# Performance work log

Hardware: AMD Instinct MI355X
Metric: run time of the kernel (lower is better)

The kernel has to match this reference:

```python
import jax, jax.numpy as jnp
import numpy as np

N_ENTITIES = 100000
N_EDGES = 500000
N_RELATIONS = 200
DIM = 64
HEADS = 4
POW_ITER = 5
ALPHA = 0.1
LEAKY_SLOPE = 0.01
EPS = 1e-16


def setup_inputs() -> dict:
    key = jax.random.key(0)
    ks = jax.random.split(key, 11)
    scale = 0.1
    return {
        "entity_embed": jax.random.normal(ks[0], (N_ENTITIES, DIM), jnp.float32),
        "relation_embed": jax.random.normal(ks[1], (N_RELATIONS, DIM), jnp.float32),
        "W_h": jax.random.normal(ks[2], (DIM, HEADS * DIM), jnp.float32) * scale,
        "W_t": jax.random.normal(ks[3], (DIM, HEADS * DIM), jnp.float32) * scale,
        "W_r": jax.random.normal(ks[4], (DIM, HEADS * DIM), jnp.float32) * scale,
        "att_h": jax.random.normal(ks[5], (HEADS, DIM), jnp.float32) * scale,
        "att_t": jax.random.normal(ks[6], (HEADS, DIM), jnp.float32) * scale,
        "att_r": jax.random.normal(ks[7], (HEADS, DIM), jnp.float32) * scale,
        "W_o": jax.random.normal(ks[8], (HEADS * DIM, DIM), jnp.float32) * scale,
        "edge_index": jax.random.randint(ks[9], (2, N_EDGES), 0, N_ENTITIES, jnp.int64),
        "edge_type": jax.random.randint(ks[10], (N_EDGES,), 0, N_RELATIONS, jnp.int64),
    }


def _segment_softmax(scores, seg_ids, num_segments):
    # scores: [E, heads]; softmax over edges sharing the same seg_id, per head
    m = jax.ops.segment_max(scores, seg_ids, num_segments=num_segments)
    e = jnp.exp(scores - m[seg_ids])
    denom = jax.ops.segment_sum(e, seg_ids, num_segments=num_segments)
    return e / (denom[seg_ids] + EPS)


def reference(entity_embed, relation_embed, W_h, W_t, W_r,
              att_h, att_t, att_r, W_o, edge_index, edge_type):
    head_ids, tail_ids = edge_index[0], edge_index[1]

    # per-edge gathered embeddings, projected per head: [E, heads, dim]
    Wh = (entity_embed[head_ids] @ W_h).reshape(-1, HEADS, DIM)
    Wt = (entity_embed[tail_ids] @ W_t).reshape(-1, HEADS, DIM)
    Wr = (relation_embed[edge_type] @ W_r).reshape(-1, HEADS, DIM)

    s_h = jnp.sum(jnp.tanh(Wh) * att_h[None], axis=-1)  # [E, heads]
    s_t = jnp.sum(jnp.tanh(Wt) * att_t[None], axis=-1)
    s_r = jnp.sum(jnp.tanh(Wr) * att_r[None], axis=-1)
    scores = jax.nn.leaky_relu(s_h + s_t + s_r, negative_slope=LEAKY_SLOPE)

    att = _segment_softmax(scores, head_ids, N_ENTITIES)  # [E, heads]
    A = (1.0 - ALPHA) * att

    # PPR power iteration, vectorized over heads: Z: [N, heads, dim]
    Z0 = entity_embed[:, None, :]  # [N, 1, dim]
    Z_init = jnp.broadcast_to(Z0, (N_ENTITIES, HEADS, DIM))

    def step(Z, _):
        msgs = A[:, :, None] * Z[tail_ids]  # [E, heads, dim]
        Z_new = jax.ops.segment_sum(msgs, head_ids, num_segments=N_ENTITIES) + ALPHA * Z0
        return Z_new, None

    Z, _ = jax.lax.scan(step, Z_init, None, length=POW_ITER)

    out = Z.reshape(N_ENTITIES, HEADS * DIM) @ W_o  # [N, dim]
    return out
```

## Files before the change

kernel.cpp:

```cpp
#include <hip/hip_runtime.h>
#include <hip/hip_fp16.h>
#include <math.h>

#define N_ENT 100000
#define N_EDGE 500000
#define N_REL 200

typedef short bf16x8 __attribute__((ext_vector_type(8)));
typedef _Float16 f16x8 __attribute__((ext_vector_type(8)));
typedef float f32x4 __attribute__((ext_vector_type(4)));

__device__ __forceinline__ float fast_tanh(float x) {
    float xc = fminf(x, 15.f);
    float e = __expf(2.f * xc);
    return 1.f - 2.f * __builtin_amdgcn_rcpf(e + 1.f);
}

__device__ __forceinline__ unsigned short f2bf(float f) {
    unsigned u = __float_as_uint(f);
    unsigned r = u + 0x7FFF + ((u >> 16) & 1);
    return (unsigned short)(r >> 16);
}

__device__ __forceinline__ uint2 pack_half4(const float4 v) {
    __half2 lo = __floats2half2_rn(v.x, v.y);
    __half2 hi = __floats2half2_rn(v.z, v.w);
    uint2 r;
    r.x = *reinterpret_cast<const unsigned int*>(&lo);
    r.y = *reinterpret_cast<const unsigned int*>(&hi);
    return r;
}

__device__ __forceinline__ float4 unpack_half4(uint2 u) {
    __half2 lo = *reinterpret_cast<const __half2*>(&u.x);
    __half2 hi = *reinterpret_cast<const __half2*>(&u.y);
    float2 a = __half22float2(lo);
    float2 b = __half22float2(hi);
    return make_float4(a.x, a.y, b.x, b.y);
}

__global__ __launch_bounds__(256) void cvt_emb_kernel(
    const float* __restrict__ in, unsigned short* __restrict__ out, int nquads)
{
    for (int i = blockIdx.x * 256 + threadIdx.x; i < nquads; i += gridDim.x * 256) {
        float4 v = ((const float4*)in)[i];
        ushort4 o;
        o.x = f2bf(v.x); o.y = f2bf(v.y); o.z = f2bf(v.z); o.w = f2bf(v.w);
        ((ushort4*)out)[i] = o;
    }
}

__global__ __launch_bounds__(256) void cvt_wT_kernel(
    const float* __restrict__ W0, const float* __restrict__ W1,
    unsigned short* __restrict__ wT)
{
    int idx = blockIdx.x * 256 + threadIdx.x;
    if (idx >= 2 * 256 * 64) return;
    int mat = idx >> 14;
    int rem = idx & 16383;
    int col = rem >> 6;
    int k   = rem & 63;
    const float* W = (mat == 0) ? W0 : W1;
    wT[idx] = f2bf(W[k * 256 + col]);
}

__global__ __launch_bounds__(256) void cvt_woT_kernel(
    const float* __restrict__ Wo, __half* __restrict__ woT)
{
    int idx = blockIdx.x * 256 + threadIdx.x;
    if (idx >= 64 * 256) return;
    int d = idx >> 8;
    int k = idx & 255;
    woT[idx] = __float2half(Wo[k * 64 + d]);
}

__global__ __launch_bounds__(256) void proj_mfma_kernel(
    const unsigned short* __restrict__ emb_bf,
    const unsigned short* __restrict__ wT,
    const float* __restrict__ att0, const float* __restrict__ att1,
    float* __restrict__ p0, float* __restrict__ p1, int nrows)
{
    const int wv   = threadIdx.x >> 6;
    const int lane = threadIdx.x & 63;
    const int r4   = lane >> 4;
    const int cl   = lane & 15;
    const int rowbase = blockIdx.x * 64 + wv * 16;

    int ra = min(rowbase + cl, nrows - 1);
    bf16x8 a0 = *(const bf16x8*)(emb_bf + (size_t)ra * 64 + 8 * r4);
    bf16x8 a1 = *(const bf16x8*)(emb_bf + (size_t)ra * 64 + 8 * r4 + 32);

#pragma unroll
    for (int mat = 0; mat < 2; ++mat) {
        const float* att = (mat == 0) ? att0 : att1;
        float* p         = (mat == 0) ? p0 : p1;
        float pacc[4][4];
#pragma unroll
        for (int head = 0; head < 4; ++head) {
            float vsum[4] = {0.f, 0.f, 0.f, 0.f};
#pragma unroll
            for (int sub = 0; sub < 4; ++sub) {
                int col = head * 64 + sub * 16 + cl;
                const unsigned short* wp =
                    wT + ((size_t)(mat * 256 + col)) * 64 + 8 * r4;
                bf16x8 b0 = *(const bf16x8*)(wp);
                bf16x8 b1 = *(const bf16x8*)(wp + 32);
                f32x4 c = {0.f, 0.f, 0.f, 0.f};
                c = __builtin_amdgcn_mfma_f32_16x16x32_bf16(a0, b0, c, 0, 0, 0);
                c = __builtin_amdgcn_mfma_f32_16x16x32_bf16(a1, b1, c, 0, 0, 0);
                float av = att[head * 64 + sub * 16 + cl];
#pragma unroll
                for (int j = 0; j < 4; ++j)
                    vsum[j] = fmaf(fast_tanh(c[j]), av, vsum[j]);
            }
#pragma unroll
            for (int j = 0; j < 4; ++j) {
                float v = vsum[j];
                v += __shfl_xor(v, 1, 64);
                v += __shfl_xor(v, 2, 64);
                v += __shfl_xor(v, 4, 64);
                v += __shfl_xor(v, 8, 64);
                pacc[head][j] = v;
            }
        }
        if (cl == 0) {
#pragma unroll
            for (int j = 0; j < 4; ++j) {
                int row = rowbase + r4 * 4 + j;
                if (row < nrows) {
                    *(float4*)(p + (size_t)row * 4) = make_float4(
                        pacc[0][j], pacc[1][j], pacc[2][j], pacc[3][j]);
                }
            }
        }
    }
}

__global__ __launch_bounds__(256) void proj_gemm_kernel(
    const float* __restrict__ emb,
    const float* __restrict__ W0,
    const float* __restrict__ att0,
    float* __restrict__ p0,
    int nrows)
{
    __shared__ float e_lds[64][68];
    __shared__ float w0_lds[64][64];
    __shared__ float red[4][4][64];

    const int t    = threadIdx.x;
    const int wv   = t >> 6;
    const int lane = t & 63;
    const int er   = t & 15;
    const int d0   = (t >> 4) * 4;
    const int base = blockIdx.x * 64;

#pragma unroll
    for (int i = 0; i < 4; ++i) {
        int f = t + 256 * i;
        int row = f >> 4, c4 = f & 15;
        int gr = min(base + row, nrows - 1);
        float4 v = *(const float4*)(emb + (size_t)gr * 64 + 4 * c4);
        *(float4*)&e_lds[row][4 * c4] = v;
    }

    float p0s[4][4];

    for (int head = 0; head < 4; ++head) {
        {
            int k0 = t >> 4, c4 = t & 15;
#pragma unroll
            for (int kk = 0; kk < 4; ++kk) {
                int k = k0 + 16 * kk;
                *(float4*)&w0_lds[k][4 * c4] =
                    *(const float4*)(W0 + (size_t)k * 256 + head * 64 + 4 * c4);
            }
        }
        __syncthreads();

        float acc0[4][4] = {};
        for (int k4 = 0; k4 < 16; ++k4) {
            float4 z0 = *(const float4*)&e_lds[er +  0][4 * k4];
            float4 z1 = *(const float4*)&e_lds[er + 16][4 * k4];
            float4 z2 = *(const float4*)&e_lds[er + 32][4 * k4];
            float4 z3 = *(const float4*)&e_lds[er + 48][4 * k4];
            const float zr[4][4] = {
                {z0.x, z0.y, z0.z, z0.w},
                {z1.x, z1.y, z1.z, z1.w},
                {z2.x, z2.y, z2.z, z2.w},
                {z3.x, z3.y, z3.z, z3.w}};
#pragma unroll
            for (int jj = 0; jj < 4; ++jj) {
                float4 w0v = *(const float4*)&w0_lds[4 * k4 + jj][d0];
#pragma unroll
                for (int i = 0; i < 4; ++i) {
                    float zj = zr[i][jj];
                    acc0[i][0] = fmaf(zj, w0v.x, acc0[i][0]);
                    acc0[i][1] = fmaf(zj, w0v.y, acc0[i][1]);
                    acc0[i][2] = fmaf(zj, w0v.z, acc0[i][2]);
                    acc0[i][3] = fmaf(zj, w0v.w, acc0[i][3]);
                }
            }
        }

        float4 av0 = *(const float4*)(att0 + head * 64 + d0);
#pragma unroll
        for (int i = 0; i < 4; ++i) {
            float v = fast_tanh(acc0[i][0]) * av0.x
                    + fast_tanh(acc0[i][1]) * av0.y
                    + fast_tanh(acc0[i][2]) * av0.z
                    + fast_tanh(acc0[i][3]) * av0.w;
            v += __shfl_xor(v, 16, 64);
            v += __shfl_xor(v, 32, 64);
            p0s[head][i] = v;
        }
        __syncthreads();
    }

    if (lane < 16) {
#pragma unroll
        for (int h = 0; h < 4; ++h)
#pragma unroll
            for (int i = 0; i < 4; ++i)
                red[wv][h][lane + 16 * i] = p0s[h][i];
    }
    __syncthreads();
    if (t < 64) {
        int row = base + t;
        if (row < nrows) {
            float4 pv;
            pv.x = red[0][0][t] + red[1][0][t] + red[2][0][t] + red[3][0][t];
            pv.y = red[0][1][t] + red[1][1][t] + red[2][1][t] + red[3][1][t];
            pv.z = red[0][2][t] + red[1][2][t] + red[2][2][t] + red[3][2][t];
            pv.w = red[0][3][t] + red[1][3][t] + red[2][3][t] + red[3][3][t];
            *(float4*)(p0 + (size_t)row * 4) = pv;
        }
    }
}

__global__ __launch_bounds__(256) void hist_kernel(
    const int* __restrict__ eidx, int* __restrict__ counts)
{
    int e = blockIdx.x * 256 + threadIdx.x;
    if (e >= N_EDGE) return;
    atomicAdd(&counts[eidx[e]], 1);
}

__global__ __launch_bounds__(1024) void scan_kernel(
    const int* __restrict__ counts, int* __restrict__ row_start)
{
    __shared__ int wsum[16];
    __shared__ int carry_s;
    const int lane = threadIdx.x & 63;
    const int wid  = threadIdx.x >> 6;
    if (threadIdx.x == 0) carry_s = 0;
    __syncthreads();
    for (int base = 0; base < N_ENT; base += 4096) {
        int i0 = base + (int)threadIdx.x * 4;
        int4 v = make_int4(0, 0, 0, 0);
        if (i0 + 3 < N_ENT) v = *(const int4*)(counts + i0);
        else {
            if (i0 + 0 < N_ENT) v.x = counts[i0 + 0];
            if (i0 + 1 < N_ENT) v.y = counts[i0 + 1];
            if (i0 + 2 < N_ENT) v.z = counts[i0 + 2];
            if (i0 + 3 < N_ENT) v.w = counts[i0 + 3];
        }
        int s1 = v.x + v.y, s2 = s1 + v.z, tsum = s2 + v.w;
        int incl = tsum;
#pragma unroll
        for (int off = 1; off < 64; off <<= 1) {
            int t = __shfl_up(incl, off, 64);
            if (lane >= off) incl += t;
        }
        if (lane == 63) wsum[wid] = incl;
        __syncthreads();
        int wave_off = 0;
#pragma unroll
        for (int w = 0; w < 16; ++w)
            wave_off += (w < wid) ? wsum[w] : 0;
        int carry = carry_s;
        int excl = carry + wave_off + (incl - tsum);
        if (i0 + 3 < N_ENT) {
            *(int4*)(row_start + i0) = make_int4(excl, excl + v.x, excl + s1, excl + s2);
        } else {
            if (i0 + 0 < N_ENT) row_start[i0 + 0] = excl;
            if (i0 + 1 < N_ENT) row_start[i0 + 1] = excl + v.x;
            if (i0 + 2 < N_ENT) row_start[i0 + 2] = excl + s1;
            if (i0 + 3 < N_ENT) row_start[i0 + 3] = excl + s2;
        }
        __syncthreads();
        if (threadIdx.x == 1023) carry_s = carry + wave_off + incl;
    }
    __syncthreads();
    if (threadIdx.x == 0) row_start[N_ENT] = carry_s;
}

__global__ __launch_bounds__(256) void scatter_score_kernel(
    const int* __restrict__ eidx, const int* __restrict__ etype,
    const float* __restrict__ ph, const float* __restrict__ pt,
    const float* __restrict__ pr,
    const int* __restrict__ row_start, int* __restrict__ cursor,
    int* __restrict__ csr_col, float* __restrict__ csr_a)
{
    int e = blockIdx.x * 256 + threadIdx.x;
    if (e >= N_EDGE) return;
    int hn = eidx[e];
    int tn = eidx[N_EDGE + e];
    int r  = etype[e];
    float4 a = *(const float4*)(ph + (size_t)hn * 4);
    float4 b = *(const float4*)(pt + (size_t)tn * 4);
    float4 c = *(const float4*)(pr + (size_t)r * 4);
    float s0 = a.x + b.x + c.x;
    float s1 = a.y + b.y + c.y;
    float s2 = a.z + b.z + c.z;
    float s3 = a.w + b.w + c.w;
    s0 = s0 >= 0.f ? s0 : 0.01f * s0;
    s1 = s1 >= 0.f ? s1 : 0.01f * s1;
    s2 = s2 >= 0.f ? s2 : 0.01f * s2;
    s3 = s3 >= 0.f ? s3 : 0.01f * s3;
    float4 ev = make_float4(__expf(s0), __expf(s1), __expf(s2), __expf(s3));
    int pos = row_start[hn] + atomicAdd(&cursor[hn], 1);
    csr_col[pos] = tn;
    *(float4*)(csr_a + (size_t)pos * 4) = ev;
}

__global__ __launch_bounds__(256) void normalize_kernel(
    const int* __restrict__ row_start, float* __restrict__ csr_a)
{
    const int wid  = threadIdx.x >> 6;
    const int lane = threadIdx.x & 63;
    const int n = blockIdx.x * 4 + wid;
    if (n >= N_ENT) return;
    const int s   = row_start[n];
    const int end = row_start[n + 1];
    const int nf  = (end - s) * 4;

    float sum = 0.f;
    for (int f = lane; f < nf; f += 64)
        sum += csr_a[(size_t)s * 4 + f];
#pragma unroll
    for (int off = 4; off < 64; off <<= 1)
        sum += __shfl_xor(sum, off, 64);
    float scale = 0.9f * __builtin_amdgcn_rcpf(sum + 1e-16f);
    for (int f = lane; f < nf; f += 64)
        csr_a[(size_t)s * 4 + f] *= scale;
}

template <bool IN_HALF>
__device__ __forceinline__ float4 spmm_row(
    int n, int lane, int h,
    const __half* __restrict__ Zin_h, const float* __restrict__ emb,
    const int* __restrict__ row_start, const int* __restrict__ csr_col,
    const float* __restrict__ csr_a)
{
    const float4* e4 = (const float4*)emb;
    float4 zi = e4[(size_t)n * 16 + (lane & 15)];
    float4 acc0 = make_float4(0.1f * zi.x, 0.1f * zi.y, 0.1f * zi.z, 0.1f * zi.w);
    float4 acc1 = make_float4(0.f, 0.f, 0.f, 0.f);
    float4 acc2 = make_float4(0.f, 0.f, 0.f, 0.f);
    float4 acc3 = make_float4(0.f, 0.f, 0.f, 0.f);

    const int s   = row_start[n];
    const int end = row_start[n + 1];

    auto zrow = [&](int c) -> float4 {
        if (IN_HALF) {
            uint2 u = *(const uint2*)(Zin_h + (size_t)c * 256 + 4 * lane);
            return unpack_half4(u);
        } else {
            return *(const float4*)(emb + (size_t)c * 64 + 4 * (lane & 15));
        }
    };
    auto fma4 = [](float4& acc, float a, const float4& z) {
        acc.x = fmaf(a, z.x, acc.x);
        acc.y = fmaf(a, z.y, acc.y);
        acc.z = fmaf(a, z.z, acc.z);
        acc.w = fmaf(a, z.w, acc.w);
    };

    for (int b = s; b < end; b += 16) {
        const int nb = min(16, end - b);
        int   cl = (lane < nb) ? csr_col[b + lane] : 0;
        float al = (lane < nb * 4) ? csr_a[(size_t)b * 4 + lane] : 0.f;

        int j = 0;
        for (; j + 4 <= nb; j += 4) {
            int c0 = __shfl(cl, j + 0, 64);
            int c1 = __shfl(cl, j + 1, 64);
            int c2 = __shfl(cl, j + 2, 64);
            int c3 = __shfl(cl, j + 3, 64);
            float a0 = __shfl(al, (j + 0) * 4 + h, 64);
            float a1 = __shfl(al, (j + 1) * 4 + h, 64);
            float a2 = __shfl(al, (j + 2) * 4 + h, 64);
            float a3 = __shfl(al, (j + 3) * 4 + h, 64);
            float4 za = zrow(c0);
            float4 zb = zrow(c1);
            float4 zc = zrow(c2);
            float4 zd = zrow(c3);
            fma4(acc0, a0, za);
            fma4(acc1, a1, zb);
            fma4(acc2, a2, zc);
            fma4(acc3, a3, zd);
        }
        if (j + 0 < nb) {
            int c = __shfl(cl, j + 0, 64);
            float a = __shfl(al, (j + 0) * 4 + h, 64);
            fma4(acc0, a, zrow(c));
        }
        if (j + 1 < nb) {
            int c = __shfl(cl, j + 1, 64);
            float a = __shfl(al, (j + 1) * 4 + h, 64);
            fma4(acc1, a, zrow(c));
        }
        if (j + 2 < nb) {
            int c = __shfl(cl, j + 2, 64);
            float a = __shfl(al, (j + 2) * 4 + h, 64);
            fma4(acc2, a, zrow(c));
        }
    }
    acc0.x += acc1.x + acc2.x + acc3.x;
    acc0.y += acc1.y + acc2.y + acc3.y;
    acc0.z += acc1.z + acc2.z + acc3.z;
    acc0.w += acc1.w + acc2.w + acc3.w;
    return acc0;
}

template <bool IN_HALF>
__global__ __launch_bounds__(256) void spmm_kernel(
    const void* __restrict__ Zin_v, const float* __restrict__ emb,
    const int* __restrict__ row_start, const int* __restrict__ csr_col,
    const float* __restrict__ csr_a, void* __restrict__ Zout_v)
{
    const int wave = threadIdx.x >> 6;
    const int lane = threadIdx.x & 63;
    const int n = blockIdx.x * 4 + wave;
    const int h = lane >> 4;
    float4 acc = spmm_row<IN_HALF>(n, lane, h, (const __half*)Zin_v, emb,
                                   row_start, csr_col, csr_a);
    *(uint2*)((__half*)Zout_v + (size_t)n * 256 + 4 * lane) = pack_half4(acc);
}

__global__ __launch_bounds__(256) void spmm_out_fused_kernel(
    const __half* __restrict__ Zin, const float* __restrict__ emb,
    const int* __restrict__ row_start, const int* __restrict__ csr_col,
    const float* __restrict__ csr_a,
    const __half* __restrict__ woT,
    float* __restrict__ out)
{
    __shared__ _Float16 zl[16][264];
    const int wv   = threadIdx.x >> 6;
    const int lane = threadIdx.x & 63;
    const int h    = lane >> 4;
    const int base = blockIdx.x * 16;

#pragma unroll
    for (int rr = 0; rr < 4; ++rr) {
        int n = base + wv * 4 + rr;
        float4 acc = spmm_row<true>(n, lane, h, Zin, emb,
                                    row_start, csr_col, csr_a);
        *(uint2*)&zl[wv * 4 + rr][4 * lane] = pack_half4(acc);
    }
    __syncthreads();

    const int cl = lane & 15;
    const int r4 = lane >> 4;
    f16x8 a[8];
#pragma unroll
    for (int ks = 0; ks < 8; ++ks)
        a[ks] = *(const f16x8*)&zl[cl][ks * 32 + 8 * r4];

    const _Float16* wcol = (const _Float16*)woT + (size_t)(wv * 16 + cl) * 256 + 8 * r4;
    f32x4 c = {0.f, 0.f, 0.f, 0.f};
#pragma unroll
    for (int ks = 0; ks < 8; ++ks) {
        f16x8 b = *(const f16x8*)(wcol + ks * 32);
        c = __builtin_amdgcn_mfma_f32_16x16x32_f16(a[ks], b, c, 0, 0, 0);
    }
#pragma unroll
    for (int j = 0; j < 4; ++j) {
        int row = base + r4 * 4 + j;
        out[(size_t)row * 64 + wv * 16 + cl] = c[j];
    }
}

extern "C" void kernel_launch(void* const* d_in, const int* in_sizes, int n_in,
                              void* d_out, int out_size, void* d_ws, size_t ws_size,
                              hipStream_t stream)
{
    const float* entity = (const float*)d_in[0];
    const float* rel    = (const float*)d_in[1];
    const float* W_h    = (const float*)d_in[2];
    const float* W_t    = (const float*)d_in[3];
    const float* W_r    = (const float*)d_in[4];
    const float* att_h  = (const float*)d_in[5];
    const float* att_t  = (const float*)d_in[6];
    const float* att_r  = (const float*)d_in[7];
    const float* W_o    = (const float*)d_in[8];
    const int*   eidx   = (const int*)d_in[9];
    const int*   etype  = (const int*)d_in[10];
    float* out = (float*)d_out;

    char* ws = (char*)d_ws;
    size_t off = 0;
    auto alloc = [&](size_t bytes) -> void* {
        void* p = ws + off;
        off += (bytes + 255) & ~(size_t)255;
        return p;
    };
    float* p_h      = (float*)alloc((size_t)N_ENT * 4 * 4);
    float* p_t      = (float*)alloc((size_t)N_ENT * 4 * 4);
    float* p_r      = (float*)alloc((size_t)N_REL * 4 * 4);
    int*   counts   = (int*)alloc((size_t)N_ENT * 4);
    int*   row_start= (int*)alloc(((size_t)N_ENT + 1) * 4);
    int*   cursor   = (int*)alloc((size_t)N_ENT * 4);
    int*   csr_col  = (int*)alloc((size_t)N_EDGE * 4);
    float* csr_a    = (float*)alloc((size_t)N_EDGE * 4 * 4);
    __half* Zh_a    = (__half*)alloc((size_t)N_ENT * 256 * 2);
    __half* Zh_b    = (__half*)alloc((size_t)N_ENT * 256 * 2);
    unsigned short* emb_bf = (unsigned short*)alloc((size_t)N_ENT * 64 * 2);
    unsigned short* wT     = (unsigned short*)alloc((size_t)2 * 256 * 64 * 2);
    __half* woT     = (__half*)alloc((size_t)64 * 256 * 2);

    hipMemsetAsync(counts, 0, (size_t)N_ENT * 4, stream);
    hipMemsetAsync(cursor, 0, (size_t)N_ENT * 4, stream);

    cvt_emb_kernel<<<2048, 256, 0, stream>>>(entity, emb_bf, N_ENT * 64 / 4);
    cvt_wT_kernel<<<(2 * 256 * 64 + 255) / 256, 256, 0, stream>>>(W_h, W_t, wT);
    cvt_woT_kernel<<<(64 * 256 + 255) / 256, 256, 0, stream>>>(W_o, woT);

    proj_mfma_kernel<<<(N_ENT + 63) / 64, 256, 0, stream>>>(
        emb_bf, wT, att_h, att_t, p_h, p_t, N_ENT);
    proj_gemm_kernel<<<(N_REL + 63) / 64, 256, 0, stream>>>(
        rel, W_r, att_r, p_r, N_REL);

    hist_kernel<<<(N_EDGE + 255) / 256, 256, 0, stream>>>(eidx, counts);
    scan_kernel<<<1, 1024, 0, stream>>>(counts, row_start);
    scatter_score_kernel<<<(N_EDGE + 255) / 256, 256, 0, stream>>>(
        eidx, etype, p_h, p_t, p_r, row_start, cursor, csr_col, csr_a);
    normalize_kernel<<<(N_ENT + 3) / 4, 256, 0, stream>>>(row_start, csr_a);

    spmm_kernel<false><<<N_ENT / 4, 256, 0, stream>>>(nullptr, entity, row_start, csr_col, csr_a, Zh_b);
    spmm_kernel<true ><<<N_ENT / 4, 256, 0, stream>>>(Zh_b, entity, row_start, csr_col, csr_a, Zh_a);
    spmm_kernel<true ><<<N_ENT / 4, 256, 0, stream>>>(Zh_a, entity, row_start, csr_col, csr_a, Zh_b);
    spmm_kernel<true ><<<N_ENT / 4, 256, 0, stream>>>(Zh_b, entity, row_start, csr_col, csr_a, Zh_a);
    spmm_out_fused_kernel<<<N_ENT / 16, 256, 0, stream>>>(
        Zh_a, entity, row_start, csr_col, csr_a, woT, out);
}
```

Baseline: 439.4 us.

## Fuse prep kernels with histogram, split projection grid, fuse normalize into first SpMM

Merges the embedding/weight conversion kernels and the edge histogram into one block-partitioned prep kernel. The head/tail projection kernel is split across twice as many blocks, one per matrix, for more parallelism. The softmax normalization is folded into the first power-iteration SpMM, which rescales and writes back csr_a while accumulating, removing one kernel launch and one pass over the edge weights. This trades fewer launches and less memory traffic for more branchy kernels and extra code paths.

```diff
diff --git a/kernel.cpp b/kernel.cpp
--- a/kernel.cpp
+++ b/kernel.cpp
@@ -39,98 +39,103 @@
     return make_float4(a.x, a.y, b.x, b.y);
 }
 
-__global__ __launch_bounds__(256) void cvt_emb_kernel(
-    const float* __restrict__ in, unsigned short* __restrict__ out, int nquads)
-{
-    for (int i = blockIdx.x * 256 + threadIdx.x; i < nquads; i += gridDim.x * 256) {
-        float4 v = ((const float4*)in)[i];
-        ushort4 o;
-        o.x = f2bf(v.x); o.y = f2bf(v.y); o.z = f2bf(v.z); o.w = f2bf(v.w);
-        ((ushort4*)out)[i] = o;
-    }
-}
-
-__global__ __launch_bounds__(256) void cvt_wT_kernel(
+#define HIST_B 1954
+#define EMB_B  2048
+#define WT_B   128
+#define WOT_B  64
+__global__ __launch_bounds__(256) void prep_kernel(
+    const float* __restrict__ entity, unsigned short* __restrict__ emb_bf,
     const float* __restrict__ W0, const float* __restrict__ W1,
-    unsigned short* __restrict__ wT)
-{
-    int idx = blockIdx.x * 256 + threadIdx.x;
-    if (idx >= 2 * 256 * 64) return;
-    int mat = idx >> 14;
-    int rem = idx & 16383;
-    int col = rem >> 6;
-    int k   = rem & 63;
-    const float* W = (mat == 0) ? W0 : W1;
-    wT[idx] = f2bf(W[k * 256 + col]);
-}
-
-__global__ __launch_bounds__(256) void cvt_woT_kernel(
-    const float* __restrict__ Wo, __half* __restrict__ woT)
-{
-    int idx = blockIdx.x * 256 + threadIdx.x;
-    if (idx >= 64 * 256) return;
-    int d = idx >> 8;
-    int k = idx & 255;
-    woT[idx] = __float2half(Wo[k * 64 + d]);
+    unsigned short* __restrict__ wT,
+    const float* __restrict__ Wo, __half* __restrict__ woT,
+    const int* __restrict__ eidx, int* __restrict__ counts)
+{
+    int bid = blockIdx.x;
+    if (bid < HIST_B) {
+        int e = bid * 256 + threadIdx.x;
+        if (e < N_EDGE) atomicAdd(&counts[eidx[e]], 1);
+    } else if (bid < HIST_B + EMB_B) {
+        int b = bid - HIST_B;
+        const int nquads = N_ENT * 64 / 4;
+        for (int i = b * 256 + threadIdx.x; i < nquads; i += EMB_B * 256) {
+            float4 v = ((const float4*)entity)[i];
+            ushort4 o;
+            o.x = f2bf(v.x); o.y = f2bf(v.y); o.z = f2bf(v.z); o.w = f2bf(v.w);
+            ((ushort4*)emb_bf)[i] = o;
+        }
+    } else if (bid < HIST_B + EMB_B + WT_B) {
+        int idx = (bid - HIST_B - EMB_B) * 256 + threadIdx.x;
+        int mat = idx >> 14;
+        int rem = idx & 16383;
+        int col = rem >> 6;
+        int k   = rem & 63;
+        const float* W = (mat == 0) ? W0 : W1;
+        wT[idx] = f2bf(W[k * 256 + col]);
+    } else {
+        int idx = (bid - HIST_B - EMB_B - WT_B) * 256 + threadIdx.x;
+        int d = idx >> 8;
+        int k = idx & 255;
+        woT[idx] = __float2half(Wo[k * 64 + d]);
+    }
 }
 
 __global__ __launch_bounds__(256) void proj_mfma_kernel(
     const unsigned short* __restrict__ emb_bf,
     const unsigned short* __restrict__ wT,
     const float* __restrict__ att0, const float* __restrict__ att1,
-    float* __restrict__ p0, float* __restrict__ p1, int nrows)
-{
+    float* __restrict__ p0, float* __restrict__ p1, int nrows, int nb)
+{
+    const int mat = (blockIdx.x >= nb) ? 1 : 0;
+    const int rb  = blockIdx.x - mat * nb;
+    const float* att = (mat == 0) ? att0 : att1;
+    float* p         = (mat == 0) ? p0 : p1;
+    const unsigned short* wbase = wT + (size_t)mat * 256 * 64;
+
     const int wv   = threadIdx.x >> 6;
     const int lane = threadIdx.x & 63;
     const int r4   = lane >> 4;
     const int cl   = lane & 15;
-    const int rowbase = blockIdx.x * 64 + wv * 16;
+    const int rowbase = rb * 64 + wv * 16;
 
     int ra = min(rowbase + cl, nrows - 1);
     bf16x8 a0 = *(const bf16x8*)(emb_bf + (size_t)ra * 64 + 8 * r4);
     bf16x8 a1 = *(const bf16x8*)(emb_bf + (size_t)ra * 64 + 8 * r4 + 32);
 
-#pragma unroll
-    for (int mat = 0; mat < 2; ++mat) {
-        const float* att = (mat == 0) ? att0 : att1;
-        float* p         = (mat == 0) ? p0 : p1;
-        float pacc[4][4];
-#pragma unroll
-        for (int head = 0; head < 4; ++head) {
-            float vsum[4] = {0.f, 0.f, 0.f, 0.f};
-#pragma unroll
-            for (int sub = 0; sub < 4; ++sub) {
-                int col = head * 64 + sub * 16 + cl;
-                const unsigned short* wp =
-                    wT + ((size_t)(mat * 256 + col)) * 64 + 8 * r4;
-                bf16x8 b0 = *(const bf16x8*)(wp);
-                bf16x8 b1 = *(const bf16x8*)(wp + 32);
-                f32x4 c = {0.f, 0.f, 0.f, 0.f};
-                c = __builtin_amdgcn_mfma_f32_16x16x32_bf16(a0, b0, c, 0, 0, 0);
-                c = __builtin_amdgcn_mfma_f32_16x16x32_bf16(a1, b1, c, 0, 0, 0);
-                float av = att[head * 64 + sub * 16 + cl];
-#pragma unroll
-                for (int j = 0; j < 4; ++j)
-                    vsum[j] = fmaf(fast_tanh(c[j]), av, vsum[j]);
-            }
-#pragma unroll
-            for (int j = 0; j < 4; ++j) {
-                float v = vsum[j];
-                v += __shfl_xor(v, 1, 64);
-                v += __shfl_xor(v, 2, 64);
-                v += __shfl_xor(v, 4, 64);
-                v += __shfl_xor(v, 8, 64);
-                pacc[head][j] = v;
-            }
-        }
-        if (cl == 0) {
-#pragma unroll
-            for (int j = 0; j < 4; ++j) {
-                int row = rowbase + r4 * 4 + j;
-                if (row < nrows) {
-                    *(float4*)(p + (size_t)row * 4) = make_float4(
-                        pacc[0][j], pacc[1][j], pacc[2][j], pacc[3][j]);
-                }
+    float pacc[4][4];
+#pragma unroll
+    for (int head = 0; head < 4; ++head) {
+        float vsum[4] = {0.f, 0.f, 0.f, 0.f};
+#pragma unroll
+        for (int sub = 0; sub < 4; ++sub) {
+            int col = head * 64 + sub * 16 + cl;
+            const unsigned short* wp = wbase + (size_t)col * 64 + 8 * r4;
+            bf16x8 b0 = *(const bf16x8*)(wp);
+            bf16x8 b1 = *(const bf16x8*)(wp + 32);
+            f32x4 c = {0.f, 0.f, 0.f, 0.f};
+            c = __builtin_amdgcn_mfma_f32_16x16x32_bf16(a0, b0, c, 0, 0, 0);
+            c = __builtin_amdgcn_mfma_f32_16x16x32_bf16(a1, b1, c, 0, 0, 0);
+            float av = att[head * 64 + sub * 16 + cl];
+#pragma unroll
+            for (int j = 0; j < 4; ++j)
+                vsum[j] = fmaf(fast_tanh(c[j]), av, vsum[j]);
+        }
+#pragma unroll
+        for (int j = 0; j < 4; ++j) {
+            float v = vsum[j];
+            v += __shfl_xor(v, 1, 64);
+            v += __shfl_xor(v, 2, 64);
+            v += __shfl_xor(v, 4, 64);
+            v += __shfl_xor(v, 8, 64);
+            pacc[head][j] = v;
+        }
+    }
+    if (cl == 0) {
+#pragma unroll
+        for (int j = 0; j < 4; ++j) {
+            int row = rowbase + r4 * 4 + j;
+            if (row < nrows) {
+                *(float4*)(p + (size_t)row * 4) = make_float4(
+                    pacc[0][j], pacc[1][j], pacc[2][j], pacc[3][j]);
             }
         }
     }
@@ -235,14 +240,6 @@
             *(float4*)(p0 + (size_t)row * 4) = pv;
         }
     }
-}
-
-__global__ __launch_bounds__(256) void hist_kernel(
-    const int* __restrict__ eidx, int* __restrict__ counts)
-{
-    int e = blockIdx.x * 256 + threadIdx.x;
-    if (e >= N_EDGE) return;
-    atomicAdd(&counts[eidx[e]], 1);
 }
 
 __global__ __launch_bounds__(1024) void scan_kernel(
@@ -323,13 +320,15 @@
     *(float4*)(csr_a + (size_t)pos * 4) = ev;
 }
 
-__global__ __launch_bounds__(256) void normalize_kernel(
-    const int* __restrict__ row_start, float* __restrict__ csr_a)
-{
-    const int wid  = threadIdx.x >> 6;
+__global__ __launch_bounds__(256) void norm_spmm1_kernel(
+    const float* __restrict__ emb,
+    const int* __restrict__ row_start, const int* __restrict__ csr_col,
+    float* __restrict__ csr_a, __half* __restrict__ Zout)
+{
+    const int wave = threadIdx.x >> 6;
     const int lane = threadIdx.x & 63;
-    const int n = blockIdx.x * 4 + wid;
-    if (n >= N_ENT) return;
+    const int n = blockIdx.x * 4 + wave;
+    const int h = lane >> 4;
     const int s   = row_start[n];
     const int end = row_start[n + 1];
     const int nf  = (end - s) * 4;
@@ -341,17 +340,7 @@
     for (int off = 4; off < 64; off <<= 1)
         sum += __shfl_xor(sum, off, 64);
     float scale = 0.9f * __builtin_amdgcn_rcpf(sum + 1e-16f);
-    for (int f = lane; f < nf; f += 64)
-        csr_a[(size_t)s * 4 + f] *= scale;
-}
-
-template <bool IN_HALF>
-__device__ __forceinline__ float4 spmm_row(
-    int n, int lane, int h,
-    const __half* __restrict__ Zin_h, const float* __restrict__ emb,
-    const int* __restrict__ row_start, const int* __restrict__ csr_col,
-    const float* __restrict__ csr_a)
-{
+
     const float4* e4 = (const float4*)emb;
     float4 zi = e4[(size_t)n * 16 + (lane & 15)];
     float4 acc0 = make_float4(0.1f * zi.x, 0.1f * zi.y, 0.1f * zi.z, 0.1f * zi.w);
@@ -359,16 +348,84 @@
     float4 acc2 = make_float4(0.f, 0.f, 0.f, 0.f);
     float4 acc3 = make_float4(0.f, 0.f, 0.f, 0.f);
 
+    auto zrow = [&](int c) -> float4 {
+        return *(const float4*)(emb + (size_t)c * 64 + 4 * (lane & 15));
+    };
+    auto fma4 = [](float4& acc, float a, const float4& z) {
+        acc.x = fmaf(a, z.x, acc.x);
+        acc.y = fmaf(a, z.y, acc.y);
+        acc.z = fmaf(a, z.z, acc.z);
+        acc.w = fmaf(a, z.w, acc.w);
+    };
+
+    for (int b = s; b < end; b += 16) {
+        const int nb = min(16, end - b);
+        int   cl = (lane < nb) ? csr_col[b + lane] : 0;
+        float al = (lane < nb * 4) ? csr_a[(size_t)b * 4 + lane] : 0.f;
+        float aln = al * scale;
+        if (lane < nb * 4) csr_a[(size_t)b * 4 + lane] = aln;
+
+        int j = 0;
+        for (; j + 4 <= nb; j += 4) {
+            int c0 = __shfl(cl, j + 0, 64);
+            int c1 = __shfl(cl, j + 1, 64);
+            int c2 = __shfl(cl, j + 2, 64);
+            int c3 = __shfl(cl, j + 3, 64);
+            float a0 = __shfl(aln, (j + 0) * 4 + h, 64);
+            float a1 = __shfl(aln, (j + 1) * 4 + h, 64);
+            float a2 = __shfl(aln, (j + 2) * 4 + h, 64);
+            float a3 = __shfl(aln, (j + 3) * 4 + h, 64);
+            float4 za = zrow(c0);
+            float4 zb = zrow(c1);
+            float4 zc = zrow(c2);
+            float4 zd = zrow(c3);
+            fma4(acc0, a0, za);
+            fma4(acc1, a1, zb);
+            fma4(acc2, a2, zc);
+            fma4(acc3, a3, zd);
+        }
+        if (j + 0 < nb) {
+            int c = __shfl(cl, j + 0, 64);
+            float a = __shfl(aln, (j + 0) * 4 + h, 64);
+            fma4(acc0, a, zrow(c));
+        }
+        if (j + 1 < nb) {
+            int c = __shfl(cl, j + 1, 64);
+            float a = __shfl(aln, (j + 1) * 4 + h, 64);
+            fma4(acc1, a, zrow(c));
+        }
+        if (j + 2 < nb) {
+            int c = __shfl(cl, j + 2, 64);
+            float a = __shfl(aln, (j + 2) * 4 + h, 64);
+            fma4(acc2, a, zrow(c));
+        }
+    }
+    acc0.x += acc1.x + acc2.x + acc3.x;
+    acc0.y += acc1.y + acc2.y + acc3.y;
+    acc0.z += acc1.z + acc2.z + acc3.z;
+    acc0.w += acc1.w + acc2.w + acc3.w;
+    *(uint2*)(Zout + (size_t)n * 256 + 4 * lane) = pack_half4(acc0);
+}
+
+__device__ __forceinline__ float4 spmm_row_h(
+    int n, int lane, int h,
+    const __half* __restrict__ Zin_h, const float* __restrict__ emb,
+    const int* __restrict__ row_start, const int* __restrict__ csr_col,
+    const float* __restrict__ csr_a)
+{
+    const float4* e4 = (const float4*)emb;
+    float4 zi = e4[(size_t)n * 16 + (lane & 15)];
+    float4 acc0 = make_float4(0.1f * zi.x, 0.1f * zi.y, 0.1f * zi.z, 0.1f * zi.w);
+    float4 acc1 = make_float4(0.f, 0.f, 0.f, 0.f);
+    float4 acc2 = make_float4(0.f, 0.f, 0.f, 0.f);
+    float4 acc3 = make_float4(0.f, 0.f, 0.f, 0.f);
+
     const int s   = row_start[n];
     const int end = row_start[n + 1];
 
     auto zrow = [&](int c) -> float4 {
-        if (IN_HALF) {
-            uint2 u = *(const uint2*)(Zin_h + (size_t)c * 256 + 4 * lane);
-            return unpack_half4(u);
-        } else {
-            return *(const float4*)(emb + (size_t)c * 64 + 4 * (lane & 15));
-        }
+        uint2 u = *(const uint2*)(Zin_h + (size_t)c * 256 + 4 * lane);
+        return unpack_half4(u);
     };
     auto fma4 = [](float4& acc, float a, const float4& z) {
         acc.x = fmaf(a, z.x, acc.x);
@@ -424,19 +481,17 @@
     return acc0;
 }
 
-template <bool IN_HALF>
 __global__ __launch_bounds__(256) void spmm_kernel(
-    const void* __restrict__ Zin_v, const float* __restrict__ emb,
+    const __half* __restrict__ Zin, const float* __restrict__ emb,
     const int* __restrict__ row_start, const int* __restrict__ csr_col,
-    const float* __restrict__ csr_a, void* __restrict__ Zout_v)
+    const float* __restrict__ csr_a, __half* __restrict__ Zout)
 {
     const int wave = threadIdx.x >> 6;
     const int lane = threadIdx.x & 63;
     const int n = blockIdx.x * 4 + wave;
     const int h = lane >> 4;
-    float4 acc = spmm_row<IN_HALF>(n, lane, h, (const __half*)Zin_v, emb,
-                                   row_start, csr_col, csr_a);
-    *(uint2*)((__half*)Zout_v + (size_t)n * 256 + 4 * lane) = pack_half4(acc);
+    float4 acc = spmm_row_h(n, lane, h, Zin, emb, row_start, csr_col, csr_a);
+    *(uint2*)(Zout + (size_t)n * 256 + 4 * lane) = pack_half4(acc);
 }
 
 __global__ __launch_bounds__(256) void spmm_out_fused_kernel(
@@ -455,8 +510,7 @@
 #pragma unroll
     for (int rr = 0; rr < 4; ++rr) {
         int n = base + wv * 4 + rr;
-        float4 acc = spmm_row<true>(n, lane, h, Zin, emb,
-                                    row_start, csr_col, csr_a);
+        float4 acc = spmm_row_h(n, lane, h, Zin, emb, row_start, csr_col, csr_a);
         *(uint2*)&zl[wv * 4 + rr][4 * lane] = pack_half4(acc);
     }
     __syncthreads();
@@ -523,25 +577,24 @@
     hipMemsetAsync(counts, 0, (size_t)N_ENT * 4, stream);
     hipMemsetAsync(cursor, 0, (size_t)N_ENT * 4, stream);
 
-    cvt_emb_kernel<<<2048, 256, 0, stream>>>(entity, emb_bf, N_ENT * 64 / 4);
-    cvt_wT_kernel<<<(2 * 256 * 64 + 255) / 256, 256, 0, stream>>>(W_h, W_t, wT);
-    cvt_woT_kernel<<<(64 * 256 + 255) / 256, 256, 0, stream>>>(W_o, woT);
-
-    proj_mfma_kernel<<<(N_ENT + 63) / 64, 256, 0, stream>>>(
-        emb_bf, wT, att_h, att_t, p_h, p_t, N_ENT);
+    prep_kernel<<<HIST_B + EMB_B + WT_B + WOT_B, 256, 0, stream>>>(
+        entity, emb_bf, W_h, W_t, wT, W_o, woT, eidx, counts);
+
+    const int nb = (N_ENT + 63) / 64;
+    proj_mfma_kernel<<<2 * nb, 256, 0, stream>>>(
+        emb_bf, wT, att_h, att_t, p_h, p_t, N_ENT, nb);
     proj_gemm_kernel<<<(N_REL + 63) / 64, 256, 0, stream>>>(
         rel, W_r, att_r, p_r, N_REL);
 
-    hist_kernel<<<(N_EDGE + 255) / 256, 256, 0, stream>>>(eidx, counts);
     scan_kernel<<<1, 1024, 0, stream>>>(counts, row_start);
     scatter_score_kernel<<<(N_EDGE + 255) / 256, 256, 0, stream>>>(
         eidx, etype, p_h, p_t, p_r, row_start, cursor, csr_col, csr_a);
-    normalize_kernel<<<(N_ENT + 3) / 4, 256, 0, stream>>>(row_start, csr_a);
-
-    spmm_kernel<false><<<N_ENT / 4, 256, 0, stream>>>(nullptr, entity, row_start, csr_col, csr_a, Zh_b);
-    spmm_kernel<true ><<<N_ENT / 4, 256, 0, stream>>>(Zh_b, entity, row_start, csr_col, csr_a, Zh_a);
-    spmm_kernel<true ><<<N_ENT / 4, 256, 0, stream>>>(Zh_a, entity, row_start, csr_col, csr_a, Zh_b);
-    spmm_kernel<true ><<<N_ENT / 4, 256, 0, stream>>>(Zh_b, entity, row_start, csr_col, csr_a, Zh_a);
+
+    norm_spmm1_kernel<<<N_ENT / 4, 256, 0, stream>>>(
+        entity, row_start, csr_col, csr_a, Zh_b);
+    spmm_kernel<<<N_ENT / 4, 256, 0, stream>>>(Zh_b, entity, row_start, csr_col, csr_a, Zh_a);
+    spmm_kernel<<<N_ENT / 4, 256, 0, stream>>>(Zh_a, entity, row_start, csr_col, csr_a, Zh_b);
+    spmm_kernel<<<N_ENT / 4, 256, 0, stream>>>(Zh_b, entity, row_start, csr_col, csr_a, Zh_a);
     spmm_out_fused_kernel<<<N_ENT / 16, 256, 0, stream>>>(
         Zh_a, entity, row_start, csr_col, csr_a, woT, out);
 }
```

After: 415.9 us. 5.4% less time.
